# Performance work log

Measured on AMD Instinct MI355X. Metric: run time of the kernel, lower is better.

## Reference

```python
import jax, jax.numpy as jnp
import numpy as np

C_S, C_Z, H, P_QK, P_V, L = 384, 128, 12, 4, 8, 768
D = C_S // H
OUT_DIM = C_S + H * P_V * 3 + H * C_Z


def setup_inputs() -> dict:
    key = jax.random.key(0)
    ks = jax.random.split(key, 16)
    sc = lambda fan_in: 1.0 / np.sqrt(fan_in)
    inp = {
        'single': jax.random.normal(ks[0], (L, C_S), jnp.float32),
        'pair': jax.random.normal(ks[1], (L, L, C_Z), jnp.float32),
        'rots': jax.random.normal(ks[2], (L, 3, 3), jnp.float32),
        'trans': jax.random.normal(ks[3], (L, 3), jnp.float32),
        'ln_g': jnp.ones((C_S,), jnp.float32),
        'ln_b': jnp.zeros((C_S,), jnp.float32),
        'Wq': jax.random.normal(ks[4], (C_S, C_S), jnp.float32) * sc(C_S),
        'Wk': jax.random.normal(ks[5], (C_S, C_S), jnp.float32) * sc(C_S),
        'Wv': jax.random.normal(ks[6], (C_S, C_S), jnp.float32) * sc(C_S),
        'Wqp': jax.random.normal(ks[7], (C_S, H * P_QK * 3), jnp.float32) * sc(C_S),
        'bqp': jnp.zeros((H * P_QK * 3,), jnp.float32),
        'Wkp': jax.random.normal(ks[8], (C_S, H * P_QK * 3), jnp.float32) * sc(C_S),
        'bkp': jnp.zeros((H * P_QK * 3,), jnp.float32),
        'Wvp': jax.random.normal(ks[9], (C_S, H * P_V * 3), jnp.float32) * sc(C_S),
        'bvp': jnp.zeros((H * P_V * 3,), jnp.float32),
        'Wpb': jax.random.normal(ks[10], (C_Z, H), jnp.float32) * sc(C_Z),
        'head_weights': jnp.zeros((H,), jnp.float32),
        'Wo': jax.random.normal(ks[11], (OUT_DIM, C_S), jnp.float32) * sc(OUT_DIM),
        'bo': jnp.zeros((C_S,), jnp.float32),
    }
    return inp


def _layernorm(x, g, b, eps=1e-5):
    mu = x.mean(-1, keepdims=True)
    var = ((x - mu) ** 2).mean(-1, keepdims=True)
    return (x - mu) * jax.lax.rsqrt(var + eps) * g + b


def _apply_frames(pts, rots, trans):
    # pts: [L,H,P,3]; rotate each local point into global frame, then translate
    return jnp.einsum('lij,lhpj->lhpi', rots, pts) + trans[:, None, None, :]


def reference(single, pair, rots, trans, ln_g, ln_b, Wq, Wk, Wv, Wqp, bqp,
              Wkp, bkp, Wvp, bvp, Wpb, head_weights, Wo, bo):
    s = _layernorm(single, ln_g, ln_b)
    q = (s @ Wq).reshape(L, H, D)
    k = (s @ Wk).reshape(L, H, D)
    v = (s @ Wv).reshape(L, H, D)
    q_pts = (s @ Wqp + bqp).reshape(L, H, P_QK, 3)
    k_pts = (s @ Wkp + bkp).reshape(L, H, P_QK, 3)
    v_pts = (s @ Wvp + bvp).reshape(L, H, P_V, 3)

    q_g = _apply_frames(q_pts, rots, trans)
    k_g = _apply_frames(k_pts, rots, trans)
    v_g = _apply_frames(v_pts, rots, trans)

    # scalar attention logits [H, L, L]
    attn = jnp.einsum('ihd,jhd->hij', q, k) / np.sqrt(D).astype(np.float32)
    # point-distance bias: ||q_g_i - k_g_j||^2 summed over points -> [L,L,H]
    pt_diff = q_g[:, None] - k_g[None, :]            # [L,L,H,P,3]
    pt_dist_sq = (pt_diff ** 2).sum((-1, -2))        # [L,L,H]
    w_c = jax.nn.softplus(head_weights)
    attn = attn - 0.5 * w_c[:, None, None] * jnp.transpose(pt_dist_sq, (2, 0, 1))
    attn = attn + jnp.einsum('ijc,ch->hij', pair, Wpb)
    attn = jax.nn.softmax(attn, axis=-1)

    out_scalar = jnp.einsum('hij,jhd->ihd', attn, v).reshape(L, C_S)
    out_pts_g = jnp.einsum('hij,jhpc->ihpc', attn, v_g)  # [L,H,Pv,3]
    flat_pts = out_pts_g.reshape(L, H * P_V, 3) - trans[:, None, :]
    # inverse rotation = transpose: einsum with swapped rot indices
    out_pts_l = jnp.einsum('lji,lnj->lni', rots, flat_pts).reshape(L, H * P_V * 3)
    out_pair = jnp.einsum('hij,ijc->ihc', attn, pair).reshape(L, H * C_Z)

    cat = jnp.concatenate([out_scalar, out_pts_l, out_pair], axis=-1)
    return cat @ Wo + bo
```

## Files before the change

kernel.cpp:

```cpp
#include <hip/hip_runtime.h>
#include <math.h>

#define LSEQ 768
#define CS   384
#define CZ   128
#define NH   12
#define OUTD 2208
#define PROJW 1728
#define LL2  (LSEQ*LSEQ)

__device__ __forceinline__ float waveSum(float v){
#pragma unroll
  for (int o = 32; o > 0; o >>= 1) v += __shfl_down(v, o, 64);
  return v;
}

__global__ __launch_bounds__(128) void k_lnwcat(
    const float* __restrict__ x, const float* __restrict__ g,
    const float* __restrict__ b, float* __restrict__ s,
    const float* __restrict__ Wq, const float* __restrict__ Wk,
    const float* __restrict__ Wv, const float* __restrict__ Wqp,
    const float* __restrict__ Wkp, const float* __restrict__ Wvp,
    const float* __restrict__ bqp, const float* __restrict__ bkp,
    const float* __restrict__ bvp,
    float* __restrict__ wcat, float* __restrict__ bcat){
  int blk = blockIdx.x, t = threadIdx.x;
  if (blk < LSEQ){
    int i = blk;
    const float* row = x + (size_t)i*CS;
    float v0 = row[t], v1 = row[t+128], v2 = row[t+256];
    float sum = v0+v1+v2;
    float sq  = v0*v0+v1*v1+v2*v2;
    float ws1 = waveSum(sum), ws2 = waveSum(sq);
    __shared__ float red[4];
    int w = t>>6, lane = t&63;
    if (lane == 0){ red[w] = ws1; red[w+2] = ws2; }
    __syncthreads();
    float mu   = (red[0]+red[1]) * (1.f/CS);
    float var  = (red[2]+red[3]) * (1.f/CS) - mu*mu;
    float rstd = rsqrtf(var + 1e-5f);
    float* o = s + (size_t)i*CS;
    o[t]     = (v0-mu)*rstd*g[t]     + b[t];
    o[t+128] = (v1-mu)*rstd*g[t+128] + b[t+128];
    o[t+256] = (v2-mu)*rstd*g[t+256] + b[t+256];
    return;
  }
  int idx = (blk - LSEQ)*128 + t;
  if (idx < PROJW){
    float bv = 0.f;
    if (idx >= 1440)      bv = bvp[idx-1440];
    else if (idx >= 1296) bv = bkp[idx-1296];
    else if (idx >= 1152) bv = bqp[idx-1152];
    bcat[idx] = bv;
  }
  if (idx >= 384*PROJW) return;
  int r = idx / PROJW, c = idx % PROJW;
  float v;
  if (c < 384)       v = Wq[r*384 + c];
  else if (c < 768)  v = Wk[r*384 + c-384];
  else if (c < 1152) v = Wv[r*384 + c-768];
  else if (c < 1296) v = Wqp[r*144 + c-1152];
  else if (c < 1440) v = Wkp[r*144 + c-1296];
  else               v = Wvp[r*288 + c-1440];
  wcat[idx] = v;
}

__global__ __launch_bounds__(256) void k_gemm(
    const float* __restrict__ A, const float* __restrict__ B,
    const float* __restrict__ bias, float* __restrict__ C,
    int M, int N, int K, int kChunk){
  __shared__ float As[16][65];
  __shared__ float Bs[16][65];
  int j0 = blockIdx.x*64, i0 = blockIdx.y*64;
  int kBeg = blockIdx.z * kChunk;
  int t = threadIdx.x, tx = t & 15, ty = t >> 4;
  int arow = t >> 2, ak = (t & 3) * 4;
  int brow = t >> 4, bcol = (t & 15) * 4;
  float acc[4][4] = {};
  for (int kb = kBeg; kb < kBeg + kChunk; kb += 16){
    float4 av = *(const float4*)(A + (size_t)(i0+arow)*K + kb + ak);
    As[ak+0][arow]=av.x; As[ak+1][arow]=av.y; As[ak+2][arow]=av.z; As[ak+3][arow]=av.w;
    float4 bv = make_float4(0.f,0.f,0.f,0.f);
    if (j0 + bcol < N) bv = *(const float4*)(B + (size_t)(kb+brow)*N + j0 + bcol);
    Bs[brow][bcol+0]=bv.x; Bs[brow][bcol+1]=bv.y; Bs[brow][bcol+2]=bv.z; Bs[brow][bcol+3]=bv.w;
    __syncthreads();
#pragma unroll
    for (int kk = 0; kk < 16; ++kk){
      float a0=As[kk][ty*4+0],a1=As[kk][ty*4+1],a2=As[kk][ty*4+2],a3=As[kk][ty*4+3];
      float b0=Bs[kk][tx*4+0],b1=Bs[kk][tx*4+1],b2=Bs[kk][tx*4+2],b3=Bs[kk][tx*4+3];
      acc[0][0]+=a0*b0; acc[0][1]+=a0*b1; acc[0][2]+=a0*b2; acc[0][3]+=a0*b3;
      acc[1][0]+=a1*b0; acc[1][1]+=a1*b1; acc[1][2]+=a1*b2; acc[1][3]+=a1*b3;
      acc[2][0]+=a2*b0; acc[2][1]+=a2*b1; acc[2][2]+=a2*b2; acc[2][3]+=a2*b3;
      acc[3][0]+=a3*b0; acc[3][1]+=a3*b1; acc[3][2]+=a3*b2; acc[3][3]+=a3*b3;
    }
    __syncthreads();
  }
  bool noSplit = (gridDim.z == 1);
#pragma unroll
  for (int r = 0; r < 4; ++r){
    int i = i0 + ty*4 + r;
#pragma unroll
    for (int c = 0; c < 4; ++c){
      int j = j0 + tx*4 + c;
      if (j < N){
        float v = acc[r][c];
        if (noSplit && bias) v += bias[j];
        C[(size_t)i*N + j] = v;
      }
    }
  }
}

__global__ __launch_bounds__(256) void k_gemmWo(
    const float* __restrict__ A, const float* __restrict__ B, float* __restrict__ C){
  __shared__ float As[8][132];
  __shared__ float Bs[8][132];
  const int j0 = blockIdx.x*128, i0 = blockIdx.y*128;
  const int kBeg = blockIdx.z*184;
  const int t = threadIdx.x;
  const int arow = t >> 1, akq = (t & 1)*4;
  const int bk = t >> 5, bn = (t & 31)*4;
  const int tx = t & 15, ty = t >> 4;
  float acc[8][8] = {};
  for (int kb = kBeg; kb < kBeg+184; kb += 8){
    float4 av = *(const float4*)(A + (size_t)(i0+arow)*OUTD + kb + akq);
    float4 bv = *(const float4*)(B + (size_t)(kb+bk)*CS + j0 + bn);
    As[akq+0][arow]=av.x; As[akq+1][arow]=av.y; As[akq+2][arow]=av.z; As[akq+3][arow]=av.w;
    *(float4*)(&Bs[bk][bn]) = bv;
    __syncthreads();
#pragma unroll
    for (int k = 0; k < 8; ++k){
      float a[8], b[8];
      *(float4*)(a)   = *(const float4*)(&As[k][ty*8]);
      *(float4*)(a+4) = *(const float4*)(&As[k][ty*8+4]);
      *(float4*)(b)   = *(const float4*)(&Bs[k][tx*8]);
      *(float4*)(b+4) = *(const float4*)(&Bs[k][tx*8+4]);
#pragma unroll
      for (int r = 0; r < 8; ++r)
#pragma unroll
        for (int c = 0; c < 8; ++c) acc[r][c] += a[r]*b[c];
    }
    __syncthreads();
  }
  float* out = C + (size_t)blockIdx.z*LSEQ*CS;
#pragma unroll
  for (int r = 0; r < 8; ++r){
    float* o = out + (size_t)(i0+ty*8+r)*CS + j0 + tx*8;
    *(float4*)(o)   = make_float4(acc[r][0],acc[r][1],acc[r][2],acc[r][3]);
    *(float4*)(o+4) = make_float4(acc[r][4],acc[r][5],acc[r][6],acc[r][7]);
  }
}

__global__ __launch_bounds__(256) void k_prep(
    float* __restrict__ proj, const float* __restrict__ rots,
    const float* __restrict__ trans, const float* __restrict__ hw,
    float* __restrict__ Qa, float* __restrict__ Ka, float* __restrict__ nrm){
  int i = blockIdx.x, t = threadIdx.x;
  __shared__ float wcl[12];
  __shared__ float qg[144], kg[144];
  if (t < 12) wcl[t] = log1pf(__expf(hw[t]));
  float* prow = proj + (size_t)i*PROJW;
  if (t < 192){
    const float* R  = rots + i*9;
    const float* tr = trans + i*3;
    int off = (t < 48) ? (1152 + t*3) : ((t < 96) ? (1296 + (t-48)*3) : (1440 + (t-96)*3));
    float x = prow[off], y = prow[off+1], z = prow[off+2];
    float gx = R[0]*x + R[1]*y + R[2]*z + tr[0];
    float gy = R[3]*x + R[4]*y + R[5]*z + tr[1];
    float gz = R[6]*x + R[7]*y + R[8]*z + tr[2];
    if (t < 48){ qg[t*3]=gx; qg[t*3+1]=gy; qg[t*3+2]=gz; }
    else if (t < 96){ int u=t-48; kg[u*3]=gx; kg[u*3+1]=gy; kg[u*3+2]=gz; }
    else { prow[off]=gx; prow[off+1]=gy; prow[off+2]=gz; }
  }
  __syncthreads();
  const float isq = 0.17677669529663687f;
  for (int idx = t; idx < 576; idx += 256){
    int h = idx/48, d = idx%48;
    float qv = 0.f, kv = 0.f;
    if (d < 32){ qv = prow[h*32 + d]*isq; kv = prow[384 + h*32 + d]; }
    else if (d < 44){ qv = qg[h*12 + (d-32)]*wcl[h]; kv = kg[h*12 + (d-32)]; }
    Qa[((size_t)h*LSEQ + i)*48 + d] = qv;
    Ka[((size_t)h*LSEQ + i)*48 + d] = kv;
  }
  if (t < 24){
    int h = t % 12; int isK = (t >= 12) ? 1 : 0;
    const float* g = isK ? kg : qg;
    float sum = 0.f;
#pragma unroll
    for (int d = 0; d < 12; ++d){ float v = g[h*12+d]; sum += v*v; }
    nrm[((size_t)(isK*12 + h))*LSEQ + i] = -0.5f*wcl[h]*sum;
  }
}

__global__ __launch_bounds__(256) void k_qkaug(
    const float* __restrict__ Qa, const float* __restrict__ Ka,
    const float* __restrict__ nrm, float* __restrict__ logits){
  int j0 = blockIdx.x*64, i0 = blockIdx.y*64, h = blockIdx.z;
  __shared__ float Qs[64*49], Ks[64*49];
  __shared__ float nq[64], nk[64];
  int t = threadIdx.x;
  for (int idx = t; idx < 768; idx += 256){
    int row = idx/12, c4 = (idx%12)*4;
    float4 qv = *(const float4*)(Qa + ((size_t)h*LSEQ + i0+row)*48 + c4);
    Qs[row*49+c4]=qv.x; Qs[row*49+c4+1]=qv.y; Qs[row*49+c4+2]=qv.z; Qs[row*49+c4+3]=qv.w;
    float4 kv = *(const float4*)(Ka + ((size_t)h*LSEQ + j0+row)*48 + c4);
    Ks[row*49+c4]=kv.x; Ks[row*49+c4+1]=kv.y; Ks[row*49+c4+2]=kv.z; Ks[row*49+c4+3]=kv.w;
  }
  if (t < 64) nq[t] = nrm[(size_t)h*LSEQ + i0 + t];
  else if (t < 128) nk[t-64] = nrm[(size_t)(12+h)*LSEQ + j0 + (t-64)];
  __syncthreads();
  int tx = t & 15, ty = t >> 4;
  float acc[4][4] = {};
#pragma unroll 4
  for (int k = 0; k < 44; ++k){
    float a0=Qs[(ty*4+0)*49+k], a1=Qs[(ty*4+1)*49+k], a2=Qs[(ty*4+2)*49+k], a3=Qs[(ty*4+3)*49+k];
    float b0=Ks[(tx*4+0)*49+k], b1=Ks[(tx*4+1)*49+k], b2=Ks[(tx*4+2)*49+k], b3=Ks[(tx*4+3)*49+k];
    acc[0][0]+=a0*b0; acc[0][1]+=a0*b1; acc[0][2]+=a0*b2; acc[0][3]+=a0*b3;
    acc[1][0]+=a1*b0; acc[1][1]+=a1*b1; acc[1][2]+=a1*b2; acc[1][3]+=a1*b3;
    acc[2][0]+=a2*b0; acc[2][1]+=a2*b1; acc[2][2]+=a2*b2; acc[2][3]+=a2*b3;
    acc[3][0]+=a3*b0; acc[3][1]+=a3*b1; acc[3][2]+=a3*b2; acc[3][3]+=a3*b3;
  }
  float nqa[4] = {nq[ty*4], nq[ty*4+1], nq[ty*4+2], nq[ty*4+3]};
  float nk0=nk[tx*4], nk1=nk[tx*4+1], nk2=nk[tx*4+2], nk3=nk[tx*4+3];
#pragma unroll
  for (int r = 0; r < 4; ++r){
    float4 o = make_float4(acc[r][0]+nqa[r]+nk0, acc[r][1]+nqa[r]+nk1,
                           acc[r][2]+nqa[r]+nk2, acc[r][3]+nqa[r]+nk3);
    *(float4*)(logits + ((size_t)h*LSEQ + i0+ty*4+r)*LSEQ + j0 + tx*4) = o;
  }
}

__global__ __launch_bounds__(256) void k_pairfused(
    const float* __restrict__ pair, const float* __restrict__ Wpb,
    float* __restrict__ attn,
    float* __restrict__ cat){
  const int i = blockIdx.x, t = threadIdx.x;
  __shared__ __align__(16) float Sb[12*776];
  const float4* prowf4 = (const float4*)(pair + (size_t)i*LSEQ*CZ);
  const int w = t >> 6, lane = t & 63;

  float* lg0 = attn + (size_t)(w*3+0)*LL2 + (size_t)i*LSEQ;
  float* lg1 = attn + (size_t)(w*3+1)*LL2 + (size_t)i*LSEQ;
  float* lg2 = attn + (size_t)(w*3+2)*LL2 + (size_t)i*LSEQ;
  float4 X00 = *(const float4*)(lg0 + lane*4);
  float4 X01 = *(const float4*)(lg0 + 256 + lane*4);
  float4 X02 = *(const float4*)(lg0 + 512 + lane*4);
  float4 X10 = *(const float4*)(lg1 + lane*4);
  float4 X11 = *(const float4*)(lg1 + 256 + lane*4);
  float4 X12 = *(const float4*)(lg1 + 512 + lane*4);
  float4 X20 = *(const float4*)(lg2 + lane*4);
  float4 X21 = *(const float4*)(lg2 + 256 + lane*4);
  float4 X22 = *(const float4*)(lg2 + 512 + lane*4);

  for (int rr = 0; rr < 3; ++rr){
    const int r = t + rr*256;
    const float4* src = prowf4 + (size_t)r*32;
    float acc[12] = {0.f,0.f,0.f,0.f,0.f,0.f,0.f,0.f,0.f,0.f,0.f,0.f};
#pragma unroll 8
    for (int c4 = 0; c4 < 32; ++c4){
      float4 pv = src[c4];
      const float* wq = Wpb + c4*48;
#pragma unroll
      for (int h = 0; h < 12; ++h)
        acc[h] += pv.x*wq[h] + pv.y*wq[h+12] + pv.z*wq[h+24] + pv.w*wq[h+36];
    }
#pragma unroll
    for (int h = 0; h < 12; ++h) Sb[h*776 + r] = acc[h];
  }
  __syncthreads();

#pragma unroll
  for (int e = 0; e < 3; ++e){
    const int h = w*3 + e;
    float* lg = (e == 0) ? lg0 : ((e == 1) ? lg1 : lg2);
    float4 xa = (e == 0) ? X00 : ((e == 1) ? X10 : X20);
    float4 xb = (e == 0) ? X01 : ((e == 1) ? X11 : X21);
    float4 xc = (e == 0) ? X02 : ((e == 1) ? X12 : X22);
    float4 ba = *(const float4*)(Sb + h*776 + lane*4);
    float4 bb = *(const float4*)(Sb + h*776 + 256 + lane*4);
    float4 bc = *(const float4*)(Sb + h*776 + 512 + lane*4);
    xa.x+=ba.x; xa.y+=ba.y; xa.z+=ba.z; xa.w+=ba.w;
    xb.x+=bb.x; xb.y+=bb.y; xb.z+=bb.z; xb.w+=bb.w;
    xc.x+=bc.x; xc.y+=bc.y; xc.z+=bc.z; xc.w+=bc.w;
    float m = fmaxf(fmaxf(fmaxf(xa.x,xa.y),fmaxf(xa.z,xa.w)),
             fmaxf(fmaxf(fmaxf(xb.x,xb.y),fmaxf(xb.z,xb.w)),
                   fmaxf(fmaxf(xc.x,xc.y),fmaxf(xc.z,xc.w))));
#pragma unroll
    for (int ms = 32; ms > 0; ms >>= 1) m = fmaxf(m, __shfl_xor(m, ms));
    xa.x=__expf(xa.x-m); xa.y=__expf(xa.y-m); xa.z=__expf(xa.z-m); xa.w=__expf(xa.w-m);
    xb.x=__expf(xb.x-m); xb.y=__expf(xb.y-m); xb.z=__expf(xb.z-m); xb.w=__expf(xb.w-m);
    xc.x=__expf(xc.x-m); xc.y=__expf(xc.y-m); xc.z=__expf(xc.z-m); xc.w=__expf(xc.w-m);
    float s = xa.x+xa.y+xa.z+xa.w + xb.x+xb.y+xb.z+xb.w + xc.x+xc.y+xc.z+xc.w;
#pragma unroll
    for (int ms = 32; ms > 0; ms >>= 1) s += __shfl_xor(s, ms);
    float inv = 1.f/s;
    xa.x*=inv; xa.y*=inv; xa.z*=inv; xa.w*=inv;
    xb.x*=inv; xb.y*=inv; xb.z*=inv; xb.w*=inv;
    xc.x*=inv; xc.y*=inv; xc.z*=inv; xc.w*=inv;
    *(float4*)(Sb + h*776 + lane*4)       = xa;
    *(float4*)(Sb + h*776 + 256 + lane*4) = xb;
    *(float4*)(Sb + h*776 + 512 + lane*4) = xc;
    *(float4*)(lg + lane*4)       = xa;
    *(float4*)(lg + 256 + lane*4) = xb;
    *(float4*)(lg + 512 + lane*4) = xc;
  }
  __syncthreads();

  const int cq = t & 31, rp = t >> 5;
  float4 acc3[12];
#pragma unroll
  for (int h = 0; h < 12; ++h) acc3[h] = make_float4(0.f,0.f,0.f,0.f);
#pragma unroll 2
  for (int g = 0; g < 24; ++g){
    const int r0 = g*32 + rp*4;
    float4 pv0 = prowf4[(size_t)(r0+0)*32 + cq];
    float4 pv1 = prowf4[(size_t)(r0+1)*32 + cq];
    float4 pv2 = prowf4[(size_t)(r0+2)*32 + cq];
    float4 pv3 = prowf4[(size_t)(r0+3)*32 + cq];
#pragma unroll
    for (int h = 0; h < 12; ++h){
      float4 p4 = *(const float4*)(Sb + h*776 + r0);
      acc3[h].x += pv0.x*p4.x + pv1.x*p4.y + pv2.x*p4.z + pv3.x*p4.w;
      acc3[h].y += pv0.y*p4.x + pv1.y*p4.y + pv2.y*p4.z + pv3.y*p4.w;
      acc3[h].z += pv0.z*p4.x + pv1.z*p4.y + pv2.z*p4.z + pv3.z*p4.w;
      acc3[h].w += pv0.w*p4.x + pv1.w*p4.y + pv2.w*p4.z + pv3.w*p4.w;
    }
  }
#pragma unroll
  for (int h = 0; h < 12; ++h){
    acc3[h].x += __shfl_xor(acc3[h].x, 32);
    acc3[h].y += __shfl_xor(acc3[h].y, 32);
    acc3[h].z += __shfl_xor(acc3[h].z, 32);
    acc3[h].w += __shfl_xor(acc3[h].w, 32);
  }
  __syncthreads();
  if (lane < 32){
#pragma unroll
    for (int h = 0; h < 12; ++h)
      *(float4*)(Sb + w*1536 + h*128 + cq*4) = acc3[h];
  }
  __syncthreads();
  float* crow = cat + (size_t)i*OUTD + 672;
  for (int o = t; o < 1536; o += 256)
    crow[o] = Sb[o] + Sb[1536+o] + Sb[3072+o] + Sb[4608+o];
}

__global__ __launch_bounds__(256) void k_pv(
    const float* __restrict__ attn, const float* __restrict__ proj,
    const float* __restrict__ rots, const float* __restrict__ trans,
    float* __restrict__ cat){
  int h = blockIdx.y, i0 = blockIdx.x*16;
  __shared__ float As[32][17];
  __shared__ float Bs[32][57];
  __shared__ float pts[16][24];
  int t = threadIdx.x, tx = t & 15, ty = t >> 4;
  float acc[4] = {};
  for (int kb = 0; kb < LSEQ; kb += 32){
    __syncthreads();
    {
      int row = t >> 4, k2 = (t & 15)*2;
      float2 av = *(const float2*)(attn + ((size_t)h*LSEQ + i0 + row)*LSEQ + kb + k2);
      As[k2][row] = av.x; As[k2+1][row] = av.y;
    }
    for (int idx = t; idx < 32*56; idx += 256){
      int kk = idx/56, n = idx%56;
      const float* prow = proj + (size_t)(kb+kk)*PROJW;
      Bs[kk][n] = (n < 32) ? prow[768 + h*32 + n] : prow[1440 + h*24 + (n-32)];
    }
    __syncthreads();
    if (tx < 14){
#pragma unroll
      for (int kk = 0; kk < 32; ++kk){
        float a = As[kk][ty];
        float b[4]; *(float4*)b = *(const float4*)(&Bs[kk][tx*4]);
        acc[0] += a*b[0]; acc[1] += a*b[1]; acc[2] += a*b[2]; acc[3] += a*b[3];
      }
    }
  }
  __syncthreads();
  if (tx < 14){
    int i = i0 + ty;
#pragma unroll
    for (int c = 0; c < 4; ++c){
      int n = tx*4 + c;
      if (n < 32) cat[(size_t)i*OUTD + h*32 + n] = acc[c];
      else pts[ty][n-32] = acc[c];
    }
  }
  __syncthreads();
  if (t < 128){
    int row = t >> 3, p = t & 7;
    int i = i0 + row;
    const float* R = rots + i*9; const float* tr = trans + i*3;
    float x = pts[row][p*3]   - tr[0];
    float y = pts[row][p*3+1] - tr[1];
    float z = pts[row][p*3+2] - tr[2];
    float* o = cat + (size_t)i*OUTD + 384 + h*24 + p*3;
    o[0] = R[0]*x + R[3]*y + R[6]*z;
    o[1] = R[1]*x + R[4]*y + R[7]*z;
    o[2] = R[2]*x + R[5]*y + R[8]*z;
  }
}

__global__ __launch_bounds__(256) void k_reduce(
    const float* __restrict__ part, const float* __restrict__ bias,
    float* __restrict__ out){
  int idx = blockIdx.x*256 + threadIdx.x;
  if (idx >= LSEQ*CS) return;
  float v = bias[idx % CS];
#pragma unroll
  for (int z = 0; z < 12; ++z) v += part[(size_t)z*LSEQ*CS + idx];
  out[idx] = v;
}

extern "C" void kernel_launch(void* const* d_in, const int* in_sizes, int n_in,
                              void* d_out, int out_size, void* d_ws, size_t ws_size,
                              hipStream_t stream){
  const float* single = (const float*)d_in[0];
  const float* pair   = (const float*)d_in[1];
  const float* rots   = (const float*)d_in[2];
  const float* trans  = (const float*)d_in[3];
  const float* ln_g   = (const float*)d_in[4];
  const float* ln_b   = (const float*)d_in[5];
  const float* Wq  = (const float*)d_in[6];
  const float* Wk  = (const float*)d_in[7];
  const float* Wv  = (const float*)d_in[8];
  const float* Wqp = (const float*)d_in[9];
  const float* bqp = (const float*)d_in[10];
  const float* Wkp = (const float*)d_in[11];
  const float* bkp = (const float*)d_in[12];
  const float* Wvp = (const float*)d_in[13];
  const float* bvp = (const float*)d_in[14];
  const float* Wpb = (const float*)d_in[15];
  const float* hw  = (const float*)d_in[16];
  const float* Wo  = (const float*)d_in[17];
  const float* bo  = (const float*)d_in[18];
  float* out = (float*)d_out;

  float* ws = (float*)d_ws;
  float* s    = ws;
  float* wcat = ws + 294912;
  float* bcat = ws + 958464;
  float* Qa   = ws;
  float* Ka   = ws + 442368;
  float* nrm  = ws + 884736;
  float* proj = ws + 960256;
  float* attn = ws + 2287360;
  float* cat  = ws + 9365248;
  float* part = attn;

  int wcatBlocks = (384*PROJW + 127)/128;
  k_lnwcat<<<LSEQ + wcatBlocks, 128, 0, stream>>>(single, ln_g, ln_b, s,
      Wq, Wk, Wv, Wqp, Wkp, Wvp, bqp, bkp, bvp, wcat, bcat);
  k_gemm<<<dim3(27,12,1), 256, 0, stream>>>(s, wcat, bcat, proj, 768, PROJW, 384, 384);
  k_prep<<<LSEQ, 256, 0, stream>>>(proj, rots, trans, hw, Qa, Ka, nrm);
  k_qkaug<<<dim3(12,12,12), 256, 0, stream>>>(Qa, Ka, nrm, attn);
  k_pairfused<<<LSEQ, 256, 0, stream>>>(pair, Wpb, attn, cat);
  k_pv<<<dim3(48, NH), 256, 0, stream>>>(attn, proj, rots, trans, cat);
  k_gemmWo<<<dim3(3,6,12), 256, 0, stream>>>(cat, Wo, part);
  k_reduce<<<(LSEQ*CS+255)/256, 256, 0, stream>>>(part, bo, out);
}
```

Baseline: 371.0 us.

## Stage pair rows through shared memory with coalesced loads for pair bias

The pair-bias projection in the fused pair kernel now loads 64-row tiles of the pair row into shared memory with coalesced float4 loads. Each wave then computes three heads per row from LDS instead of each thread streaming its own strided row from global memory. The logits loads are moved from the kernel prologue to the softmax loop, which lowers register pressure but gives up early prefetch. The cost is extra LDS (about 33KB), more barriers, and redundant reads of each pair element from LDS by four waves.

```diff
diff --git a/kernel.cpp b/kernel.cpp
--- a/kernel.cpp
+++ b/kernel.cpp
@@ -236,46 +236,46 @@
     float* __restrict__ cat){
   const int i = blockIdx.x, t = threadIdx.x;
   __shared__ __align__(16) float Sb[12*776];
+  __shared__ __align__(16) float pairT[64*132];
   const float4* prowf4 = (const float4*)(pair + (size_t)i*LSEQ*CZ);
   const int w = t >> 6, lane = t & 63;
 
-  float* lg0 = attn + (size_t)(w*3+0)*LL2 + (size_t)i*LSEQ;
-  float* lg1 = attn + (size_t)(w*3+1)*LL2 + (size_t)i*LSEQ;
-  float* lg2 = attn + (size_t)(w*3+2)*LL2 + (size_t)i*LSEQ;
-  float4 X00 = *(const float4*)(lg0 + lane*4);
-  float4 X01 = *(const float4*)(lg0 + 256 + lane*4);
-  float4 X02 = *(const float4*)(lg0 + 512 + lane*4);
-  float4 X10 = *(const float4*)(lg1 + lane*4);
-  float4 X11 = *(const float4*)(lg1 + 256 + lane*4);
-  float4 X12 = *(const float4*)(lg1 + 512 + lane*4);
-  float4 X20 = *(const float4*)(lg2 + lane*4);
-  float4 X21 = *(const float4*)(lg2 + 256 + lane*4);
-  float4 X22 = *(const float4*)(lg2 + 512 + lane*4);
-
-  for (int rr = 0; rr < 3; ++rr){
-    const int r = t + rr*256;
-    const float4* src = prowf4 + (size_t)r*32;
-    float acc[12] = {0.f,0.f,0.f,0.f,0.f,0.f,0.f,0.f,0.f,0.f,0.f,0.f};
-#pragma unroll 8
-    for (int c4 = 0; c4 < 32; ++c4){
-      float4 pv = src[c4];
-      const float* wq = Wpb + c4*48;
-#pragma unroll
-      for (int h = 0; h < 12; ++h)
-        acc[h] += pv.x*wq[h] + pv.y*wq[h+12] + pv.z*wq[h+24] + pv.w*wq[h+36];
-    }
-#pragma unroll
-    for (int h = 0; h < 12; ++h) Sb[h*776 + r] = acc[h];
-  }
-  __syncthreads();
+  for (int tt = 0; tt < 12; ++tt){
+    const int rbase = tt*64;
+#pragma unroll
+    for (int k = 0; k < 8; ++k){
+      int u = t + k*256;
+      int row = u >> 5, cq = u & 31;
+      float4 v = prowf4[(size_t)(rbase+row)*32 + cq];
+      *(float4*)(pairT + row*132 + cq*4) = v;
+    }
+    __syncthreads();
+    {
+      float a0 = 0.f, a1 = 0.f, a2 = 0.f;
+      const float* wbase = Wpb + 3*w;
+      const float* prow = pairT + lane*132;
+#pragma unroll 4
+      for (int c4 = 0; c4 < 32; ++c4){
+        float4 pv = *(const float4*)(prow + c4*4);
+        const float* wc = wbase + c4*48;
+        a0 += pv.x*wc[0] + pv.y*wc[12] + pv.z*wc[24] + pv.w*wc[36];
+        a1 += pv.x*wc[1] + pv.y*wc[13] + pv.z*wc[25] + pv.w*wc[37];
+        a2 += pv.x*wc[2] + pv.y*wc[14] + pv.z*wc[26] + pv.w*wc[38];
+      }
+      Sb[(3*w+0)*776 + rbase + lane] = a0;
+      Sb[(3*w+1)*776 + rbase + lane] = a1;
+      Sb[(3*w+2)*776 + rbase + lane] = a2;
+    }
+    __syncthreads();
+  }
 
 #pragma unroll
   for (int e = 0; e < 3; ++e){
     const int h = w*3 + e;
-    float* lg = (e == 0) ? lg0 : ((e == 1) ? lg1 : lg2);
-    float4 xa = (e == 0) ? X00 : ((e == 1) ? X10 : X20);
-    float4 xb = (e == 0) ? X01 : ((e == 1) ? X11 : X21);
-    float4 xc = (e == 0) ? X02 : ((e == 1) ? X12 : X22);
+    float* lg = attn + (size_t)h*LL2 + (size_t)i*LSEQ;
+    float4 xa = *(const float4*)(lg + lane*4);
+    float4 xb = *(const float4*)(lg + 256 + lane*4);
+    float4 xc = *(const float4*)(lg + 512 + lane*4);
     float4 ba = *(const float4*)(Sb + h*776 + lane*4);
     float4 bb = *(const float4*)(Sb + h*776 + 256 + lane*4);
     float4 bc = *(const float4*)(Sb + h*776 + 512 + lane*4);
```

Result: slower. 437.3 us (+17.9%).

## Vectorize shared-memory GEMM reads and switch attention buffer to row-major [i][h][j]

Applied to the files above, without the earlier changes.

Pads and transposes the shared tiles in the GEMM and QK-augmented kernels so each thread reads four A and four B values as float4 instead of scalar loads. The attention logits buffer is re-laid out from [h][i][j] to [i][h][j], and the producer, the fused softmax kernel and the PV kernel are updated to match. The softmax kernel now loads its logits after the pair projection instead of prefetching them into registers, and the pair-projection loop unroll drops from 8 to 2, which cuts register pressure. The new layout makes the softmax reads of one query row contiguous across heads but makes the per-head PV reads strided.

```diff
diff --git a/kernel.cpp b/kernel.cpp
--- a/kernel.cpp
+++ b/kernel.cpp
@@ -69,8 +69,8 @@
     const float* __restrict__ A, const float* __restrict__ B,
     const float* __restrict__ bias, float* __restrict__ C,
     int M, int N, int K, int kChunk){
-  __shared__ float As[16][65];
-  __shared__ float Bs[16][65];
+  __shared__ float As[16][68];
+  __shared__ float Bs[16][68];
   int j0 = blockIdx.x*64, i0 = blockIdx.y*64;
   int kBeg = blockIdx.z * kChunk;
   int t = threadIdx.x, tx = t & 15, ty = t >> 4;
@@ -82,16 +82,17 @@
     As[ak+0][arow]=av.x; As[ak+1][arow]=av.y; As[ak+2][arow]=av.z; As[ak+3][arow]=av.w;
     float4 bv = make_float4(0.f,0.f,0.f,0.f);
     if (j0 + bcol < N) bv = *(const float4*)(B + (size_t)(kb+brow)*N + j0 + bcol);
-    Bs[brow][bcol+0]=bv.x; Bs[brow][bcol+1]=bv.y; Bs[brow][bcol+2]=bv.z; Bs[brow][bcol+3]=bv.w;
+    *(float4*)(&Bs[brow][bcol]) = bv;
     __syncthreads();
 #pragma unroll
     for (int kk = 0; kk < 16; ++kk){
-      float a0=As[kk][ty*4+0],a1=As[kk][ty*4+1],a2=As[kk][ty*4+2],a3=As[kk][ty*4+3];
-      float b0=Bs[kk][tx*4+0],b1=Bs[kk][tx*4+1],b2=Bs[kk][tx*4+2],b3=Bs[kk][tx*4+3];
-      acc[0][0]+=a0*b0; acc[0][1]+=a0*b1; acc[0][2]+=a0*b2; acc[0][3]+=a0*b3;
-      acc[1][0]+=a1*b0; acc[1][1]+=a1*b1; acc[1][2]+=a1*b2; acc[1][3]+=a1*b3;
-      acc[2][0]+=a2*b0; acc[2][1]+=a2*b1; acc[2][2]+=a2*b2; acc[2][3]+=a2*b3;
-      acc[3][0]+=a3*b0; acc[3][1]+=a3*b1; acc[3][2]+=a3*b2; acc[3][3]+=a3*b3;
+      float a[4], b[4];
+      *(float4*)a = *(const float4*)(&As[kk][ty*4]);
+      *(float4*)b = *(const float4*)(&Bs[kk][tx*4]);
+#pragma unroll
+      for (int r = 0; r < 4; ++r)
+#pragma unroll
+        for (int c = 0; c < 4; ++c) acc[r][c] += a[r]*b[c];
     }
     __syncthreads();
   }
@@ -196,15 +197,15 @@
     const float* __restrict__ Qa, const float* __restrict__ Ka,
     const float* __restrict__ nrm, float* __restrict__ logits){
   int j0 = blockIdx.x*64, i0 = blockIdx.y*64, h = blockIdx.z;
-  __shared__ float Qs[64*49], Ks[64*49];
+  __shared__ float Qs[48][68], Ks[48][68];
   __shared__ float nq[64], nk[64];
   int t = threadIdx.x;
   for (int idx = t; idx < 768; idx += 256){
     int row = idx/12, c4 = (idx%12)*4;
     float4 qv = *(const float4*)(Qa + ((size_t)h*LSEQ + i0+row)*48 + c4);
-    Qs[row*49+c4]=qv.x; Qs[row*49+c4+1]=qv.y; Qs[row*49+c4+2]=qv.z; Qs[row*49+c4+3]=qv.w;
+    Qs[c4+0][row]=qv.x; Qs[c4+1][row]=qv.y; Qs[c4+2][row]=qv.z; Qs[c4+3][row]=qv.w;
     float4 kv = *(const float4*)(Ka + ((size_t)h*LSEQ + j0+row)*48 + c4);
-    Ks[row*49+c4]=kv.x; Ks[row*49+c4+1]=kv.y; Ks[row*49+c4+2]=kv.z; Ks[row*49+c4+3]=kv.w;
+    Ks[c4+0][row]=kv.x; Ks[c4+1][row]=kv.y; Ks[c4+2][row]=kv.z; Ks[c4+3][row]=kv.w;
   }
   if (t < 64) nq[t] = nrm[(size_t)h*LSEQ + i0 + t];
   else if (t < 128) nk[t-64] = nrm[(size_t)(12+h)*LSEQ + j0 + (t-64)];
@@ -213,12 +214,13 @@
   float acc[4][4] = {};
 #pragma unroll 4
   for (int k = 0; k < 44; ++k){
-    float a0=Qs[(ty*4+0)*49+k], a1=Qs[(ty*4+1)*49+k], a2=Qs[(ty*4+2)*49+k], a3=Qs[(ty*4+3)*49+k];
-    float b0=Ks[(tx*4+0)*49+k], b1=Ks[(tx*4+1)*49+k], b2=Ks[(tx*4+2)*49+k], b3=Ks[(tx*4+3)*49+k];
-    acc[0][0]+=a0*b0; acc[0][1]+=a0*b1; acc[0][2]+=a0*b2; acc[0][3]+=a0*b3;
-    acc[1][0]+=a1*b0; acc[1][1]+=a1*b1; acc[1][2]+=a1*b2; acc[1][3]+=a1*b3;
-    acc[2][0]+=a2*b0; acc[2][1]+=a2*b1; acc[2][2]+=a2*b2; acc[2][3]+=a2*b3;
-    acc[3][0]+=a3*b0; acc[3][1]+=a3*b1; acc[3][2]+=a3*b2; acc[3][3]+=a3*b3;
+    float a[4], b[4];
+    *(float4*)a = *(const float4*)(&Qs[k][ty*4]);
+    *(float4*)b = *(const float4*)(&Ks[k][tx*4]);
+#pragma unroll
+    for (int r = 0; r < 4; ++r)
+#pragma unroll
+      for (int c = 0; c < 4; ++c) acc[r][c] += a[r]*b[c];
   }
   float nqa[4] = {nq[ty*4], nq[ty*4+1], nq[ty*4+2], nq[ty*4+3]};
   float nk0=nk[tx*4], nk1=nk[tx*4+1], nk2=nk[tx*4+2], nk3=nk[tx*4+3];
@@ -226,7 +228,7 @@
   for (int r = 0; r < 4; ++r){
     float4 o = make_float4(acc[r][0]+nqa[r]+nk0, acc[r][1]+nqa[r]+nk1,
                            acc[r][2]+nqa[r]+nk2, acc[r][3]+nqa[r]+nk3);
-    *(float4*)(logits + ((size_t)h*LSEQ + i0+ty*4+r)*LSEQ + j0 + tx*4) = o;
+    *(float4*)(logits + ((size_t)(i0+ty*4+r)*NH + h)*LSEQ + j0 + tx*4) = o;
   }
 }
 
@@ -239,24 +241,11 @@
   const float4* prowf4 = (const float4*)(pair + (size_t)i*LSEQ*CZ);
   const int w = t >> 6, lane = t & 63;
 
-  float* lg0 = attn + (size_t)(w*3+0)*LL2 + (size_t)i*LSEQ;
-  float* lg1 = attn + (size_t)(w*3+1)*LL2 + (size_t)i*LSEQ;
-  float* lg2 = attn + (size_t)(w*3+2)*LL2 + (size_t)i*LSEQ;
-  float4 X00 = *(const float4*)(lg0 + lane*4);
-  float4 X01 = *(const float4*)(lg0 + 256 + lane*4);
-  float4 X02 = *(const float4*)(lg0 + 512 + lane*4);
-  float4 X10 = *(const float4*)(lg1 + lane*4);
-  float4 X11 = *(const float4*)(lg1 + 256 + lane*4);
-  float4 X12 = *(const float4*)(lg1 + 512 + lane*4);
-  float4 X20 = *(const float4*)(lg2 + lane*4);
-  float4 X21 = *(const float4*)(lg2 + 256 + lane*4);
-  float4 X22 = *(const float4*)(lg2 + 512 + lane*4);
-
   for (int rr = 0; rr < 3; ++rr){
     const int r = t + rr*256;
     const float4* src = prowf4 + (size_t)r*32;
     float acc[12] = {0.f,0.f,0.f,0.f,0.f,0.f,0.f,0.f,0.f,0.f,0.f,0.f};
-#pragma unroll 8
+#pragma unroll 2
     for (int c4 = 0; c4 < 32; ++c4){
       float4 pv = src[c4];
       const float* wq = Wpb + c4*48;
@@ -272,10 +261,10 @@
 #pragma unroll
   for (int e = 0; e < 3; ++e){
     const int h = w*3 + e;
-    float* lg = (e == 0) ? lg0 : ((e == 1) ? lg1 : lg2);
-    float4 xa = (e == 0) ? X00 : ((e == 1) ? X10 : X20);
-    float4 xb = (e == 0) ? X01 : ((e == 1) ? X11 : X21);
-    float4 xc = (e == 0) ? X02 : ((e == 1) ? X12 : X22);
+    float* lg = attn + ((size_t)i*NH + h)*LSEQ;
+    float4 xa = *(const float4*)(lg + lane*4);
+    float4 xb = *(const float4*)(lg + 256 + lane*4);
+    float4 xc = *(const float4*)(lg + 512 + lane*4);
     float4 ba = *(const float4*)(Sb + h*776 + lane*4);
     float4 bb = *(const float4*)(Sb + h*776 + 256 + lane*4);
     float4 bc = *(const float4*)(Sb + h*776 + 512 + lane*4);
@@ -290,10 +279,10 @@
     xa.x=__expf(xa.x-m); xa.y=__expf(xa.y-m); xa.z=__expf(xa.z-m); xa.w=__expf(xa.w-m);
     xb.x=__expf(xb.x-m); xb.y=__expf(xb.y-m); xb.z=__expf(xb.z-m); xb.w=__expf(xb.w-m);
     xc.x=__expf(xc.x-m); xc.y=__expf(xc.y-m); xc.z=__expf(xc.z-m); xc.w=__expf(xc.w-m);
-    float s = xa.x+xa.y+xa.z+xa.w + xb.x+xb.y+xb.z+xb.w + xc.x+xc.y+xc.z+xc.w;
-#pragma unroll
-    for (int ms = 32; ms > 0; ms >>= 1) s += __shfl_xor(s, ms);
-    float inv = 1.f/s;
+    float sm = xa.x+xa.y+xa.z+xa.w + xb.x+xb.y+xb.z+xb.w + xc.x+xc.y+xc.z+xc.w;
+#pragma unroll
+    for (int ms = 32; ms > 0; ms >>= 1) sm += __shfl_xor(sm, ms);
+    float inv = 1.f/sm;
     xa.x*=inv; xa.y*=inv; xa.z*=inv; xa.w*=inv;
     xb.x*=inv; xb.y*=inv; xb.z*=inv; xb.w*=inv;
     xc.x*=inv; xc.y*=inv; xc.z*=inv; xc.w*=inv;
@@ -351,7 +340,7 @@
     float* __restrict__ cat){
   int h = blockIdx.y, i0 = blockIdx.x*16;
   __shared__ float As[32][17];
-  __shared__ float Bs[32][57];
+  __shared__ float Bs[32][60];
   __shared__ float pts[16][24];
   int t = threadIdx.x, tx = t & 15, ty = t >> 4;
   float acc[4] = {};
@@ -359,7 +348,7 @@
     __syncthreads();
     {
       int row = t >> 4, k2 = (t & 15)*2;
-      float2 av = *(const float2*)(attn + ((size_t)h*LSEQ + i0 + row)*LSEQ + kb + k2);
+      float2 av = *(const float2*)(attn + ((size_t)(i0+row)*NH + h)*LSEQ + kb + k2);
       As[k2][row] = av.x; As[k2+1][row] = av.y;
     }
     for (int idx = t; idx < 32*56; idx += 256){
```

After: 339.3 us. 8.6% less time.
